# Performance work log

Hardware: AMD Instinct MI355X
Metric: run time of the kernel (lower is better)

The kernel has to match this reference:

```python
import jax, jax.numpy as jnp
import numpy as np
from jax import lax

B, C, N, NB = 64, 512, 1024, 4
BC = C // NB
KS = [3, 5, 7, 9]
LEVEL = 2  # min(2, pywt.dwt_max_level(1024, 8)) = 2
FL = 8  # db4 filter length
DN = ('NCH', 'OIH', 'NCH')
# pywt db4 decomposition filters
DEC_LO = jnp.array([-0.010597401784997278, 0.032883011666982945, 0.030841381835986965,
                    -0.18703481171888114, -0.02798376941698385, 0.6308807679295904,
                    0.7148465705525415, 0.23037781330885523], jnp.float32)
DEC_HI = jnp.array([-0.23037781330885523, 0.7148465705525415, -0.6308807679295904,
                    -0.02798376941698385, 0.18703481171888114, 0.030841381835986965,
                    -0.032883011666982945, -0.010597401784997278], jnp.float32)


def conv1d(x, w, b, pad):
    y = lax.conv_general_dilated(x, w, (1,), [(pad, pad)], dimension_numbers=DN)
    return y + b[None, :, None]


def bn_relu(x, g, beta, eps=1e-5):
    # BatchNorm1d in train mode: batch statistics over (B, L) per channel
    mu = x.mean(axis=(0, 2), keepdims=True)
    var = ((x - mu) ** 2).mean(axis=(0, 2), keepdims=True)
    xn = (x - mu) * lax.rsqrt(var + eps)
    return jax.nn.relu(xn * g[None, :, None] + beta[None, :, None])


def dwt1d(x):
    # single-level pywt-compatible DWT, symmetric mode. x: [B, C, n]
    b, c, n = x.shape
    out = (n + FL - 1) // 2
    p = 2 * (out - 1) - n + FL
    xp = jnp.pad(x, ((0, 0), (0, 0), (p // 2, p - p // 2)), mode='symmetric')
    k = jnp.stack([DEC_LO[::-1], DEC_HI[::-1]])[:, None, :]  # [2,1,FL]
    y = lax.conv_general_dilated(xp.reshape(b * c, 1, -1), k, (2,), 'VALID',
                                 dimension_numbers=DN)
    y = y.reshape(b, c, 2, out)
    return y[:, :, 0], y[:, :, 1]  # (cA, cD)


def idwt1d(lo, hi):
    # single-level inverse DWT; output length = 2*nc - FL + 2
    b, c, nc = lo.shape
    x = jnp.stack([lo, hi], axis=2).reshape(b * c, 2, nc)
    # rec filters = dec filters reversed, so flipped-for-conv == dec filters
    k = jnp.stack([DEC_LO, DEC_HI])[None, :, :]  # [1,2,FL]
    y = lax.conv_general_dilated(x, k, (1,), [(FL - 1, FL - 1)],
                                 lhs_dilation=(2,), dimension_numbers=DN)
    y = y[:, 0, FL - 2: FL - 2 + 2 * nc - FL + 2]
    return y.reshape(b, c, -1)


def decouple(x):
    # TemporalPatternDecoupling: db4 wavedec(level=2) -> reconstruct low-pass-only
    # (long term) and detail-only (short term). Torch detaches before pywt.
    x = lax.stop_gradient(x)
    n = x.shape[-1]
    a, details = x, []
    for _ in range(LEVEL):
        a, d = dwt1d(a)
        details.append(d)
    la, sa = a, jnp.zeros_like(a)
    for d in reversed(details):
        dl = d.shape[-1]
        la = idwt1d(la[..., :dl], jnp.zeros_like(d))
        sa = idwt1d(sa[..., :dl], d)
    return sa[..., :n], la[..., :n]


def setup_inputs() -> dict:
    key = jax.random.key(0)
    ks = jax.random.split(key, 32)
    s = 0.05
    inp = {
        'x': jax.random.normal(ks[0], (B, C, N), jnp.float32),
        'w_init': jax.random.normal(ks[1], (C, C, 1), jnp.float32) * s,
        'b_init': jnp.zeros((C,), jnp.float32),
        'w_pf': jax.random.normal(ks[2], (BC, 2 * BC, 1), jnp.float32) * s,
        'b_pf': jnp.zeros((BC,), jnp.float32),
        'w_fus': jax.random.normal(ks[3], (C, C, 1), jnp.float32) * s,
        'b_fus': jnp.zeros((C,), jnp.float32),
    }
    for i in range(NB):
        inp[f'w_b{i + 1}'] = jax.random.normal(ks[4 + i], (BC, BC, KS[i]), jnp.float32) * s
        inp[f'b_b{i + 1}'] = jnp.zeros((BC,), jnp.float32)
        inp[f'g_b{i + 1}'] = jnp.ones((BC,), jnp.float32)
        inp[f'be_b{i + 1}'] = jnp.zeros((BC,), jnp.float32)
    return inp


def reference(x, w_init, b_init, w_b1, b_b1, g_b1, be_b1, w_b2, b_b2, g_b2, be_b2,
              w_b3, b_b3, g_b3, be_b3, w_b4, b_b4, g_b4, be_b4, w_pf, b_pf,
              w_fus, b_fus):
    identity = x
    h = conv1d(x, w_init, b_init, 0)
    branch_in = jnp.split(h, NB, axis=1)
    wb = [w_b1, w_b2, w_b3, w_b4]
    bb = [b_b1, b_b2, b_b3, b_b4]
    gb = [g_b1, g_b2, g_b3, g_b4]
    beb = [be_b1, be_b2, be_b3, be_b4]
    shorts, longs = [], []
    for i in range(NB):
        y = bn_relu(conv1d(branch_in[i], wb[i], bb[i], KS[i] // 2), gb[i], beb[i])
        s, l = decouple(y)
        shorts.append(s)
        longs.append(l)
    for b in range(1, NB):
        shorts[b] = shorts[b] + shorts[b - 1]
    for b in range(NB - 2, -1, -1):
        longs[b] = longs[b] + longs[b + 1]
    enhanced = [conv1d(jnp.concatenate([shorts[b], longs[b]], axis=1), w_pf, b_pf, 0)
                for b in range(NB)]
    out = conv1d(jnp.concatenate(enhanced, axis=1), w_fus, b_fus, 0)
    return out + identity
```

## Files before the change

### kernel.cpp

```cpp
#include <hip/hip_runtime.h>

typedef float  f32x4 __attribute__((ext_vector_type(4)));
typedef short  s16x8 __attribute__((ext_vector_type(8)));
typedef short  s16x4 __attribute__((ext_vector_type(4)));
typedef unsigned short u16;

struct PtrQuad { const float* p[4]; };

__constant__ float c_lo[8] = {-0.010597401784997278f, 0.032883011666982945f,
                              0.030841381835986965f, -0.18703481171888114f,
                              -0.02798376941698385f, 0.6308807679295904f,
                              0.7148465705525415f,  0.23037781330885523f};
__constant__ float c_hi[8] = {-0.23037781330885523f, 0.7148465705525415f,
                              -0.6308807679295904f, -0.02798376941698385f,
                              0.18703481171888114f, 0.030841381835986965f,
                              -0.032883011666982945f, -0.010597401784997278f};

__device__ __forceinline__ u16 f2bf(float f) {
    unsigned u = __float_as_uint(f);
    u += 0x7fffu + ((u >> 16) & 1u);
    return (u16)(u >> 16);
}
__device__ __forceinline__ float bf2f(u16 h) {
    return __uint_as_float(((unsigned)h) << 16);
}
__device__ __forceinline__ int lds_chunk(int row, int g) {
    return row * 4 + (g ^ ((row >> 1) & 3));
}
__device__ __forceinline__ void gload16(void* lds, const void* g) {
    __builtin_amdgcn_global_load_lds(
        (__attribute__((address_space(1))) const void*)g,
        (__attribute__((address_space(3))) void*)lds,
        16, 0, 0);
}
__device__ __forceinline__ void pipe_wait2(int t, int nt) {
    if (t + 1 < nt) asm volatile("s_waitcnt vmcnt(4)" ::: "memory");
    else            asm volatile("s_waitcnt vmcnt(0)" ::: "memory");
    __builtin_amdgcn_s_barrier();
    __builtin_amdgcn_sched_barrier(0);
}
__device__ __forceinline__ void pipe_endbar() {
    __builtin_amdgcn_sched_barrier(0);
    __builtin_amdgcn_s_barrier();
}

__global__ __launch_bounds__(256) void gemm_nt_k(
    const u16* __restrict__ A, long aB, int lda,
    const u16* __restrict__ B, long bB, int ldb,
    int K,
    u16* __restrict__ D, long dB, int dj,
    const float* __restrict__ bias)
{
    __shared__ s16x8 As[2 * 512];
    __shared__ s16x8 Bs[2 * 512];
    int flat = blockIdx.x + 8 * (blockIdx.y + 4 * blockIdx.z);
    int swz = (flat & 7) * 256 + (flat >> 3);
    const int j0 = (swz & 7) * 128;
    const int i0 = ((swz >> 3) & 3) * 128;
    const long bb = swz >> 5;
    const u16* Ab = A + bb * aB;
    const u16* Bb = B + bb * bB;
    const int tid = threadIdx.x;
    const int srow = tid >> 2, sg = tid & 3;
    const int ssg = sg ^ ((srow >> 1) & 3);
    const int l = tid & 63, w = tid >> 6;
    const int wi = (w >> 1) * 64, wj = (w & 1) * 64;
    const int lr = l & 15, lg = l >> 4;
    const long aoff0 = (long)(i0 + srow) * lda + ssg * 8;
    const long aoff1 = (long)(i0 + srow + 64) * lda + ssg * 8;
    const long boff0 = (long)(j0 + srow) * ldb + ssg * 8;
    const long boff1 = (long)(j0 + srow + 64) * ldb + ssg * 8;
    const int nt = K >> 5;
    auto stage = [&](int buf, int t) {
        const int k0 = t << 5;
        char* a0 = (char*)As + buf * 8192 + w * 1024;
        char* b0 = (char*)Bs + buf * 8192 + w * 1024;
        gload16(a0, Ab + aoff0 + k0);
        gload16(a0 + 4096, Ab + aoff1 + k0);
        gload16(b0, Bb + boff0 + k0);
        gload16(b0 + 4096, Bb + boff1 + k0);
    };
    f32x4 acc[4][4] = {};
    stage(0, 0);
    for (int t = 0; t < nt; ++t) {
        const int cur = t & 1;
        if (t + 1 < nt) stage(cur ^ 1, t + 1);
        pipe_wait2(t, nt);
        s16x8 af[4], bf[4];
        #pragma unroll
        for (int f = 0; f < 4; ++f) {
            af[f] = As[cur * 512 + lds_chunk(wi + f * 16 + lr, lg)];
            bf[f] = Bs[cur * 512 + lds_chunk(wj + f * 16 + lr, lg)];
        }
        __builtin_amdgcn_s_setprio(1);
        #pragma unroll
        for (int fi = 0; fi < 4; ++fi)
            #pragma unroll
            for (int fj = 0; fj < 4; ++fj)
                acc[fi][fj] = __builtin_amdgcn_mfma_f32_16x16x32_bf16(af[fi], bf[fj], acc[fi][fj], 0, 0, 0);
        __builtin_amdgcn_s_setprio(0);
        pipe_endbar();
    }
    u16* Db = D + bb * dB;
    #pragma unroll
    for (int fi = 0; fi < 4; ++fi) {
        const int i = i0 + wi + fi * 16 + lg * 4;
        float b0 = 0, b1 = 0, b2v = 0, b3 = 0;
        if (bias) { b0 = bias[i]; b1 = bias[i + 1]; b2v = bias[i + 2]; b3 = bias[i + 3]; }
        #pragma unroll
        for (int fj = 0; fj < 4; ++fj) {
            const int j = j0 + wj + fj * 16 + lr;
            f32x4 d = acc[fi][fj];
            s16x4 o;
            o[0] = (short)f2bf(d[0] + b0); o[1] = (short)f2bf(d[1] + b1);
            o[2] = (short)f2bf(d[2] + b2v); o[3] = (short)f2bf(d[3] + b3);
            *(s16x4*)(Db + (long)j * dj + i) = o;
        }
    }
}

__global__ __launch_bounds__(256) void gemm_branch4_k(
    const u16* __restrict__ WpAll,
    const u16* __restrict__ H,
    u16* __restrict__ Y,
    const u16* __restrict__ zbuf,
    float* __restrict__ part)
{
    __shared__ char Alds[2 * 8192];
    __shared__ char Blds[2 * 12288];
    __shared__ float sred[2][128];
    __shared__ float qred[2][128];
    int flat = blockIdx.x + 8 * (blockIdx.y + 4 * blockIdx.z);
    int swz = (flat & 7) * 256 + (flat >> 3);
    const int jblk = swz & 7;
    const int br = (swz >> 3) & 3;
    const long bb = swz >> 5;
    const int j0 = jblk * 128;
    const int taps = 3 + 2 * br;
    const int pad = 1 + br;
    const u16* Wpb = WpAll + (long)(br * br + 2 * br) * 16384;
    const u16* Hb = H + bb * 524288 + 128 * br;
    const int tid = threadIdx.x;
    const int l = tid & 63, w = tid >> 6;
    const int wi = (w >> 1) * 64, wj = (w & 1) * 64;
    const int lr = l & 15, lg = l >> 4;
    const int lrow = l >> 2, lq = l & 3;
    const int ssg2 = lq ^ ((lrow >> 1) & 3);
    const int lda = taps * 128;

    auto stageA = [&](int buf, int c, int t) {
        char* dst = Alds + buf * 8192 + w * 2048;
        #pragma unroll
        for (int q = 0; q < 2; ++q) {
            int row = w * 32 + q * 16 + lrow;
            gload16(dst + q * 1024,
                    Wpb + (long)row * lda + t * 128 + c * 32 + ssg2 * 8);
        }
    };
    auto stageB = [&](int buf, int c) {
        char* dst = Blds + buf * 12288 + w * 3072;
        #pragma unroll
        for (int q = 0; q < 3; ++q) {
            int winrow = w * 48 + q * 16 + lrow;
            int grow = j0 - 32 + winrow;
            const u16* src = (grow >= 0 && grow < 1024)
                           ? (Hb + (long)grow * 512 + c * 32 + ssg2 * 8) : zbuf;
            gload16(dst + q * 1024, src);
        }
    };

    f32x4 acc[4][4] = {};
    int abuf = 0, bbuf = 0;
    stageB(0, 0);
    stageA(0, 0, 0);
    for (int c = 0; c < 4; ++c) {
        for (int t = 0; t < taps; ++t) {
            if (t + 1 < taps) {
                stageA(abuf ^ 1, c, t + 1);
                asm volatile("s_waitcnt vmcnt(2)" ::: "memory");
            } else if (c + 1 < 4) {
                stageB(bbuf ^ 1, c + 1);
                stageA(abuf ^ 1, c + 1, 0);
                asm volatile("s_waitcnt vmcnt(5)" ::: "memory");
            } else {
                asm volatile("s_waitcnt vmcnt(0)" ::: "memory");
            }
            __builtin_amdgcn_s_barrier();
            __builtin_amdgcn_sched_barrier(0);
            const char* Al = Alds + abuf * 8192;
            const char* Bl = Blds + bbuf * 12288;
            const int shift2 = t - pad + 32;
            s16x8 af[4], bf[4];
            #pragma unroll
            for (int f = 0; f < 4; ++f) {
                int arow = wi + f * 16 + lr;
                af[f] = *(const s16x8*)(Al + arow * 64 + (lg ^ ((arow >> 1) & 3)) * 16);
                int brow = wj + f * 16 + lr + shift2;
                bf[f] = *(const s16x8*)(Bl + brow * 64 + (lg ^ ((brow >> 1) & 3)) * 16);
            }
            __builtin_amdgcn_s_setprio(1);
            #pragma unroll
            for (int fi = 0; fi < 4; ++fi)
                #pragma unroll
                for (int fj = 0; fj < 4; ++fj)
                    acc[fi][fj] = __builtin_amdgcn_mfma_f32_16x16x32_bf16(af[fi], bf[fj], acc[fi][fj], 0, 0, 0);
            __builtin_amdgcn_s_setprio(0);
            __builtin_amdgcn_sched_barrier(0);
            __builtin_amdgcn_s_barrier();
            abuf ^= 1;
            if (t == taps - 1) bbuf ^= 1;
        }
    }
    u16* Db = Y + bb * 524288 + 128 * br;
    #pragma unroll
    for (int fi = 0; fi < 4; ++fi) {
        const int i = wi + fi * 16 + lg * 4;
        #pragma unroll
        for (int fj = 0; fj < 4; ++fj) {
            const int j = j0 + wj + fj * 16 + lr;
            f32x4 d = acc[fi][fj];
            s16x4 o;
            o[0] = (short)f2bf(d[0]); o[1] = (short)f2bf(d[1]);
            o[2] = (short)f2bf(d[2]); o[3] = (short)f2bf(d[3]);
            *(s16x4*)(Db + (long)j * 512 + i) = o;
        }
    }
    float sv[16], qv[16];
    #pragma unroll
    for (int fi = 0; fi < 4; ++fi)
        #pragma unroll
        for (int e = 0; e < 4; ++e) {
            float s = 0.f, q = 0.f;
            #pragma unroll
            for (int fj = 0; fj < 4; ++fj) { float d = acc[fi][fj][e]; s += d; q += d * d; }
            sv[fi * 4 + e] = s; qv[fi * 4 + e] = q;
        }
    #pragma unroll
    for (int m = 1; m < 16; m <<= 1) {
        #pragma unroll
        for (int r = 0; r < 16; ++r) {
            sv[r] += __shfl_xor(sv[r], m, 64);
            qv[r] += __shfl_xor(qv[r], m, 64);
        }
    }
    __syncthreads();
    if (lr == 0) {
        #pragma unroll
        for (int r = 0; r < 16; ++r) {
            int co = wi + (r >> 2) * 16 + lg * 4 + (r & 3);
            sred[w & 1][co] = sv[r];
            qred[w & 1][co] = qv[r];
        }
    }
    __syncthreads();
    if (tid < 128) {
        long blk = (long)br * 512 + bb * 8 + jblk;
        part[blk * 256 + tid]       = sred[0][tid] + sred[1][tid];
        part[blk * 256 + 128 + tid] = qred[0][tid] + qred[1][tid];
    }
}

__global__ __launch_bounds__(256) void gemm_psl_k(
    const u16* __restrict__ Ybn,
    const u16* __restrict__ Bmat,
    u16* __restrict__ PSL)
{
    __shared__ s16x8 As[2 * 512];
    __shared__ s16x8 Bs[2 * 512];
    int flat = blockIdx.x + 8 * (blockIdx.y + 8 * blockIdx.z);
    int swz = (flat & 7) * 512 + (flat >> 3);
    const int j0 = (swz & 7) * 128;
    const int i0 = ((swz >> 3) & 7) * 128;
    const long bb = swz >> 6;
    const int tid = threadIdx.x;
    const u16* Ab = Ybn + bb * 524288;
    const int srow = tid >> 2, sg = tid & 3;
    const int ssg = sg ^ ((srow >> 1) & 3);
    const int l = tid & 63, w = tid >> 6;
    const int wi = (w >> 1) * 64, wj = (w & 1) * 64;
    const int lr = l & 15, lg = l >> 4;
    const long aoff0 = (long)(i0 + srow) * 512 + ssg * 8;
    const long aoff1 = (long)(i0 + srow + 64) * 512 + ssg * 8;
    const long boff0 = (long)(j0 + srow) * 512 + ssg * 8;
    const long boff1 = (long)(j0 + srow + 64) * 512 + ssg * 8;
    const int nt = 16;
    auto stage = [&](int buf, int t) {
        const int k0 = t << 5;
        char* a0 = (char*)As + buf * 8192 + w * 1024;
        char* b0 = (char*)Bs + buf * 8192 + w * 1024;
        gload16(a0, Ab + aoff0 + k0);
        gload16(a0 + 4096, Ab + aoff1 + k0);
        gload16(b0, Bmat + boff0 + k0);
        gload16(b0 + 4096, Bmat + boff1 + k0);
    };
    f32x4 acc[4][4] = {};
    stage(0, 0);
    for (int t = 0; t < nt; ++t) {
        const int cur = t & 1;
        if (t + 1 < nt) stage(cur ^ 1, t + 1);
        pipe_wait2(t, nt);
        s16x8 af[4], bf[4];
        #pragma unroll
        for (int f = 0; f < 4; ++f) {
            af[f] = As[cur * 512 + lds_chunk(wi + f * 16 + lr, lg)];
            bf[f] = Bs[cur * 512 + lds_chunk(wj + f * 16 + lr, lg)];
        }
        __builtin_amdgcn_s_setprio(1);
        #pragma unroll
        for (int fi = 0; fi < 4; ++fi)
            #pragma unroll
            for (int fj = 0; fj < 4; ++fj)
                acc[fi][fj] = __builtin_amdgcn_mfma_f32_16x16x32_bf16(af[fi], bf[fj], acc[fi][fj], 0, 0, 0);
        __builtin_amdgcn_s_setprio(0);
        pipe_endbar();
    }
    u16* Db = PSL + bb * 1048576;
    #pragma unroll
    for (int fi = 0; fi < 4; ++fi) {
        const int i = i0 + wi + fi * 16 + lg * 4;
        #pragma unroll
        for (int fj = 0; fj < 4; ++fj) {
            const int j = j0 + wj + fj * 16 + lr;
            f32x4 d = acc[fi][fj];
            s16x4 o;
            o[0] = (short)f2bf(d[0]); o[1] = (short)f2bf(d[1]);
            o[2] = (short)f2bf(d[2]); o[3] = (short)f2bf(d[3]);
            *(s16x4*)(Db + (long)j * 1024 + i) = o;
        }
    }
}

__global__ __launch_bounds__(256) void gemm_time_k(
    const u16* __restrict__ MS,
    const u16* __restrict__ PSL,
    const float* __restrict__ b2, const u16* __restrict__ xbf,
    float* __restrict__ OUT)
{
    __shared__ s16x8 As[2 * 512];
    __shared__ s16x8 Bs[2 * 512];
    int flat = blockIdx.x + 4 * (blockIdx.y + 8 * blockIdx.z);
    int swz = (flat & 7) * 256 + (flat >> 3);
    const int j0 = (swz & 3) * 128;
    const int i0 = ((swz >> 2) & 7) * 128;
    const long bb = swz >> 5;
    const int tid = threadIdx.x;
    const int srow = tid >> 2, sg = tid & 3;
    const int ssg = sg ^ ((srow >> 1) & 3);
    const int l = tid & 63, w = tid >> 6;
    const int wi = (w >> 1) * 64, wj = (w & 1) * 64;
    const int lr = l & 15, lg = l >> 4;
    const int klo = (i0 - 32) > 0 ? (i0 - 32) : 0;
    const int khi = (i0 + 160) < 1024 ? (i0 + 160) : 1024;
    const int nt = (khi - klo) >> 5;
    const u16* B = PSL + bb * 1048576;
    auto stage = [&](int buf, int t) {
        const int k0 = klo + (t << 5);
        char* a0 = (char*)As + buf * 8192 + w * 1024;
        char* b0 = (char*)Bs + buf * 8192 + w * 1024;
        gload16(a0, MS + (long)(i0 + srow) * 1024 + k0 + ssg * 8);
        gload16(a0 + 4096, MS + (long)(i0 + srow + 64) * 1024 + k0 + ssg * 8);
        gload16(b0, B + (long)(j0 + srow) * 1024 + k0 + ssg * 8);
        gload16(b0 + 4096, B + (long)(j0 + srow + 64) * 1024 + k0 + ssg * 8);
    };
    f32x4 acc[4][4] = {};
    stage(0, 0);
    for (int t = 0; t < nt; ++t) {
        const int cur = t & 1;
        if (t + 1 < nt) stage(cur ^ 1, t + 1);
        pipe_wait2(t, nt);
        s16x8 af[4], bf[4];
        #pragma unroll
        for (int f = 0; f < 4; ++f) {
            af[f] = As[cur * 512 + lds_chunk(wi + f * 16 + lr, lg)];
            bf[f] = Bs[cur * 512 + lds_chunk(wj + f * 16 + lr, lg)];
        }
        __builtin_amdgcn_s_setprio(1);
        #pragma unroll
        for (int fi = 0; fi < 4; ++fi)
            #pragma unroll
            for (int fj = 0; fj < 4; ++fj)
                acc[fi][fj] = __builtin_amdgcn_mfma_f32_16x16x32_bf16(af[fi], bf[fj], acc[fi][fj], 0, 0, 0);
        __builtin_amdgcn_s_setprio(0);
        pipe_endbar();
    }
    float* Ob = OUT + bb * 524288;
    const u16* Xb = xbf + bb * 524288;
    const u16* PLb = PSL + bb * 1048576 + 524288;
    #pragma unroll
    for (int fi = 0; fi < 4; ++fi) {
        const int i = i0 + wi + fi * 16 + lg * 4;
        #pragma unroll
        for (int fj = 0; fj < 4; ++fj) {
            const int j = j0 + wj + fj * 16 + lr;
            const long a = (long)j * 1024 + i;
            f32x4 d = acc[fi][fj];
            const float bj = b2[j];
            s16x4 xv4 = *(const s16x4*)(Xb + a);
            s16x4 pl4 = *(const s16x4*)(PLb + a);
            f32x4 o;
            o[0] = d[0] + bj + bf2f((u16)xv4[0]) + bf2f((u16)pl4[0]);
            o[1] = d[1] + bj + bf2f((u16)xv4[1]) + bf2f((u16)pl4[1]);
            o[2] = d[2] + bj + bf2f((u16)xv4[2]) + bf2f((u16)pl4[2]);
            o[3] = d[3] + bj + bf2f((u16)xv4[3]) + bf2f((u16)pl4[3]);
            *(f32x4*)(Ob + a) = o;
        }
    }
}

__global__ __launch_bounds__(256) void build_M_k(u16* __restrict__ MS)
{
    __shared__ float a1[515], d1[515], a2[261], d2[261], sa1[515];
    const int r = blockIdx.x;
    const int t = threadIdx.x;
    for (int m = t; m < 515; m += 256) {
        float sa = 0.f, sd = 0.f;
        #pragma unroll
        for (int j = 0; j < 8; ++j) {
            int tt = 2 * m + 1 - j;
            tt = (tt < 0) ? (-tt - 1) : tt;
            tt = (tt >= 1024) ? (2047 - tt) : tt;
            if (tt == r) { sa += c_lo[j]; sd += c_hi[j]; }
        }
        a1[m] = sa; d1[m] = sd;
    }
    __syncthreads();
    for (int m = t; m < 261; m += 256) {
        float sa = 0.f, sd = 0.f;
        #pragma unroll
        for (int j = 0; j < 8; ++j) {
            int tt = 2 * m + 1 - j;
            tt = (tt < 0) ? (-tt - 1) : tt;
            tt = (tt >= 515) ? (1029 - tt) : tt;
            float v = a1[tt];
            sa += v * c_lo[j]; sd += v * c_hi[j];
        }
        a2[m] = sa; d2[m] = sd;
    }
    __syncthreads();
    for (int m = t; m < 515; m += 256) {
        float ss = 0.f;
        #pragma unroll
        for (int k = 0; k < 8; ++k) {
            int tt = m + k - 1;
            if (tt & 1) continue;
            int j = tt >> 1;
            if (j < 0 || j >= 261) continue;
            ss += c_hi[k] * d2[j];
        }
        sa1[m] = ss;
    }
    __syncthreads();
    for (int n = t; n < 1024; n += 256) {
        float ss = 0.f;
        #pragma unroll
        for (int k = 0; k < 8; ++k) {
            int tt = n + k - 1;
            if (tt & 1) continue;
            int j = tt >> 1;
            if (j < 0 || j >= 515) continue;
            ss += c_lo[k] * sa1[j] + c_hi[k] * d1[j];
        }
        MS[(long)n * 1024 + r] = f2bf(ss);
    }
}

__global__ __launch_bounds__(256) void pack_weights_k(
    const float* __restrict__ wi,
    const float* __restrict__ b1, const float* __restrict__ b2_,
    const float* __restrict__ b3, const float* __restrict__ b4,
    const float* __restrict__ wf, const float* __restrict__ bpf,
    const float* __restrict__ bfus,
    u16* __restrict__ Wi, u16* __restrict__ Wp,
    float* __restrict__ bias2, float* __restrict__ zbuf)
{
    int i = blockIdx.x * 256 + threadIdx.x;
    if (i < 262144) Wi[i] = f2bf(wi[i]);
    if (i < 393216) {
        int base, taps;
        const float* s;
        if (i < 49152)       { base = 0;      taps = 3; s = b1; }
        else if (i < 131072) { base = 49152;  taps = 5; s = b2_; }
        else if (i < 245760) { base = 131072; taps = 7; s = b3; }
        else                 { base = 245760; taps = 9; s = b4; }
        int rem = i - base;
        int stride = taps * 128;
        int co = rem / stride;
        int r2 = rem - co * stride;
        int tap = r2 >> 7, ci = r2 & 127;
        Wp[i] = f2bf(s[(long)(co * 128 + ci) * taps + tap]);
    }
    if (i < 512) {
        float s = bfus[i];
        for (int j = 0; j < 512; ++j) s += wf[(long)i * 512 + j] * bpf[j & 127];
        bias2[i] = s;
    }
    if (i >= 512 && i < 576) zbuf[i - 512] = 0.f;
}

__global__ __launch_bounds__(256) void make_Ucum_k(
    const float* __restrict__ wf, const float* __restrict__ wp,
    u16* __restrict__ UDUL)
{
    int gid = blockIdx.x * 256 + threadIdx.x;
    int co = gid >> 7, cc = gid & 127;
    float us[4], ul[4];
    #pragma unroll
    for (int b = 0; b < 4; ++b) {
        float s = 0.f, t = 0.f;
        for (int q = 0; q < 128; ++q) {
            float f = wf[(long)co * 512 + b * 128 + q];
            s += f * wp[q * 256 + cc];
            t += f * wp[q * 256 + 128 + cc];
        }
        us[b] = s; ul[b] = t;
    }
    float suf[4], pre[4];
    float acc = 0.f;
    for (int b = 3; b >= 0; --b) { acc += us[b]; suf[b] = acc; }
    acc = 0.f;
    for (int b = 0; b < 4; ++b) { acc += ul[b]; pre[b] = acc; }
    #pragma unroll
    for (int b = 0; b < 4; ++b) {
        UDUL[(long)co * 512 + b * 128 + cc]         = f2bf(suf[b] - pre[b]);
        UDUL[(long)(512 + co) * 512 + b * 128 + cc] = f2bf(pre[b]);
    }
}

__global__ __launch_bounds__(256) void trX_k(const float* __restrict__ x,
                                             u16* __restrict__ xcl,
                                             u16* __restrict__ xbf)
{
    __shared__ float sh[32][33];
    const int n0 = blockIdx.x * 32, c0 = blockIdx.y * 32;
    const long bb = blockIdx.z;
    const int tx = threadIdx.x, ty = threadIdx.y;
    const float* xb = x + bb * 524288;
    u16* ob = xcl + bb * 524288;
    u16* fb = xbf + bb * 524288;
    #pragma unroll
    for (int k = 0; k < 4; ++k) {
        float v = xb[(long)(c0 + ty + 8 * k) * 1024 + n0 + tx];
        sh[ty + 8 * k][tx] = v;
        fb[(long)(c0 + ty + 8 * k) * 1024 + n0 + tx] = f2bf(v);
    }
    __syncthreads();
    #pragma unroll
    for (int k = 0; k < 4; ++k)
        ob[(long)(n0 + ty + 8 * k) * 512 + c0 + tx] = f2bf(sh[tx][ty + 8 * k]);
}

__global__ __launch_bounds__(256) void bn_coef_k(
    const float* __restrict__ part, PtrQuad g, PtrQuad be, float* __restrict__ scsh)
{
    __shared__ float rs[256], rq[256];
    int c = blockIdx.x;
    int br = c >> 7, cc = c & 127;
    const float* pb = part + (long)br * 131072;
    int t = threadIdx.x;
    float s = pb[(2 * t) * 256 + cc]       + pb[(2 * t + 1) * 256 + cc];
    float q = pb[(2 * t) * 256 + 128 + cc] + pb[(2 * t + 1) * 256 + 128 + cc];
    rs[t] = s; rq[t] = q;
    __syncthreads();
    for (int off = 128; off > 0; off >>= 1) {
        if (t < off) { rs[t] += rs[t + off]; rq[t] += rq[t + off]; }
        __syncthreads();
    }
    if (t == 0) {
        float mu = rs[0] * (1.0f / 65536.0f);
        float var = rq[0] * (1.0f / 65536.0f) - mu * mu;
        float sc = g.p[br][cc] * rsqrtf(var + 1e-5f);
        scsh[c] = sc;
        scsh[512 + c] = be.p[br][cc] - mu * sc;
    }
}

__global__ __launch_bounds__(256) void bn_apply_k(
    u16* __restrict__ Y, const float* __restrict__ scsh)
{
    __shared__ float sc_[512];
    __shared__ float sh_[512];
    const int t = threadIdx.x;
    #pragma unroll
    for (int q = 0; q < 2; ++q) {
        sc_[t + q * 256] = scsh[t + q * 256];
        sh_[t + q * 256] = scsh[512 + t + q * 256];
    }
    __syncthreads();
    long gid = (long)blockIdx.x * 256 + t;
    long r = gid >> 6; int cg = (int)(gid & 63);
    u16* p = Y + r * 512 + cg * 8;
    s16x8 v = *(const s16x8*)p;
    #pragma unroll
    for (int e = 0; e < 8; ++e) {
        int c = cg * 8 + e;
        float f = bf2f((u16)v[e]) * sc_[c] + sh_[c];
        v[e] = (short)f2bf(f > 0.f ? f : 0.f);
    }
    *(s16x8*)p = v;
}

extern "C" void kernel_launch(void* const* d_in, const int* in_sizes, int n_in,
                              void* d_out, int out_size, void* d_ws, size_t ws_size,
                              hipStream_t stream)
{
    const float* x      = (const float*)d_in[0];
    const float* w_init = (const float*)d_in[1];
    const float* b_init = (const float*)d_in[2];
    const float* w_pf   = (const float*)d_in[3];
    const float* b_pf   = (const float*)d_in[4];
    const float* w_fus  = (const float*)d_in[5];
    const float* b_fus  = (const float*)d_in[6];
    const float *w_b[4];
    PtrQuad g, be;
    for (int i = 0; i < 4; ++i) {
        w_b[i]  = (const float*)d_in[7 + 4 * i];
        g.p[i]  = (const float*)d_in[9 + 4 * i];
        be.p[i] = (const float*)d_in[10 + 4 * i];
    }
    float* outf = (float*)d_out;

    char* p = (char*)d_ws;
    u16* xcl   = (u16*)p;  p += 67108864;
    u16* xbf   = (u16*)p;  p += 67108864;
    u16* h     = (u16*)p;  p += 67108864;
    u16* Y     = (u16*)p;  p += 67108864;
    u16* PSL   = (u16*)p;  p += 134217728;
    u16* Wi    = (u16*)p;  p += 524288;
    u16* Wp    = (u16*)p;  p += 786432;
    u16* UDUL  = (u16*)p;  p += 1048576;
    u16* MrowS = (u16*)p;  p += 2097152;
    float* b2  = (float*)p; p += 2048;
    float* zbuf= (float*)p; p += 256;
    float* scsh= (float*)p; p += 4096;
    float* part= (float*)p; p += 2097152;

    pack_weights_k<<<1536, 256, 0, stream>>>(w_init, w_b[0], w_b[1], w_b[2], w_b[3],
                                             w_fus, b_pf, b_fus, Wi, Wp, b2, zbuf);
    make_Ucum_k<<<256, 256, 0, stream>>>(w_fus, w_pf, UDUL);
    build_M_k<<<1024, 256, 0, stream>>>(MrowS);

    trX_k<<<dim3(32, 16, 64), dim3(32, 8), 0, stream>>>(x, xcl, xbf);

    gemm_nt_k<<<dim3(8, 4, 64), 256, 0, stream>>>(Wi, 0, 512, xcl, 524288, 512, 512,
                                                  h, 524288, 512, b_init);

    gemm_branch4_k<<<dim3(8, 4, 64), 256, 0, stream>>>(Wp, h, Y, (const u16*)zbuf, part);

    bn_coef_k<<<512, 256, 0, stream>>>(part, g, be, scsh);
    bn_apply_k<<<16384, 256, 0, stream>>>(Y, scsh);

    gemm_psl_k<<<dim3(8, 8, 64), 256, 0, stream>>>(Y, UDUL, PSL);

    gemm_time_k<<<dim3(4, 8, 64), 256, 0, stream>>>(MrowS, PSL, b2, xbf, outf);
}
```

Before: 481.0 us.

## Use 512-thread 256x128 GEMM tiles for init and PSL projections

Replaces the 128x128 256-thread GEMM with a generic 512-thread kernel that computes 256x128 output tiles, with eight waves sharing one B tile. Both the init conv GEMM and the PSL GEMM now go through this kernel, and the separate gemm_psl_k is removed. The larger tile is meant to cut global/LDS traffic per MFMA and halve the workgroup count. In exchange it uses more LDS per block, fewer workgroups for latency hiding, and a new vmcnt(3) wait scheme.

```diff
diff --git a/kernel.cpp b/kernel.cpp
--- a/kernel.cpp
+++ b/kernel.cpp
@@ -44,52 +44,60 @@
     __builtin_amdgcn_s_barrier();
 }
 
-__global__ __launch_bounds__(256) void gemm_nt_k(
+__global__ __launch_bounds__(512) void gemm_nt8_k(
     const u16* __restrict__ A, long aB, int lda,
     const u16* __restrict__ B, long bB, int ldb,
-    int K,
+    int nI, int nJ,
     u16* __restrict__ D, long dB, int dj,
     const float* __restrict__ bias)
 {
-    __shared__ s16x8 As[2 * 512];
+    __shared__ s16x8 As[2 * 1024];
     __shared__ s16x8 Bs[2 * 512];
-    int flat = blockIdx.x + 8 * (blockIdx.y + 4 * blockIdx.z);
-    int swz = (flat & 7) * 256 + (flat >> 3);
-    const int j0 = (swz & 7) * 128;
-    const int i0 = ((swz >> 3) & 3) * 128;
-    const long bb = swz >> 5;
+    int flat = blockIdx.x + gridDim.x * (blockIdx.y + gridDim.y * blockIdx.z);
+    int nwg = gridDim.x * gridDim.y * gridDim.z;
+    int swz = (flat & 7) * (nwg >> 3) + (flat >> 3);
+    const int jt = swz % nJ;
+    int rest = swz / nJ;
+    const int it = rest % nI;
+    const long bb = rest / nI;
+    const int i0 = it * 256, j0 = jt * 128;
     const u16* Ab = A + bb * aB;
     const u16* Bb = B + bb * bB;
     const int tid = threadIdx.x;
     const int srow = tid >> 2, sg = tid & 3;
     const int ssg = sg ^ ((srow >> 1) & 3);
     const int l = tid & 63, w = tid >> 6;
-    const int wi = (w >> 1) * 64, wj = (w & 1) * 64;
+    const int wi = (w >> 1) * 64;
+    const int wj = (w & 1) * 64;
     const int lr = l & 15, lg = l >> 4;
     const long aoff0 = (long)(i0 + srow) * lda + ssg * 8;
-    const long aoff1 = (long)(i0 + srow + 64) * lda + ssg * 8;
-    const long boff0 = (long)(j0 + srow) * ldb + ssg * 8;
-    const long boff1 = (long)(j0 + srow + 64) * ldb + ssg * 8;
-    const int nt = K >> 5;
+    const long aoff1 = (long)(i0 + srow + 128) * lda + ssg * 8;
+    const long boff  = (long)(j0 + srow) * ldb + ssg * 8;
+    const int nt = 16;
     auto stage = [&](int buf, int t) {
         const int k0 = t << 5;
-        char* a0 = (char*)As + buf * 8192 + w * 1024;
+        char* a0 = (char*)As + buf * 16384 + w * 1024;
         char* b0 = (char*)Bs + buf * 8192 + w * 1024;
         gload16(a0, Ab + aoff0 + k0);
-        gload16(a0 + 4096, Ab + aoff1 + k0);
-        gload16(b0, Bb + boff0 + k0);
-        gload16(b0 + 4096, Bb + boff1 + k0);
+        gload16(a0 + 8192, Ab + aoff1 + k0);
+        gload16(b0, Bb + boff + k0);
     };
     f32x4 acc[4][4] = {};
     stage(0, 0);
     for (int t = 0; t < nt; ++t) {
         const int cur = t & 1;
-        if (t + 1 < nt) stage(cur ^ 1, t + 1);
-        pipe_wait2(t, nt);
+        if (t + 1 < nt) {
+            stage(cur ^ 1, t + 1);
+            asm volatile("s_waitcnt vmcnt(3)" ::: "memory");
+        } else {
+            asm volatile("s_waitcnt vmcnt(0)" ::: "memory");
+        }
+        __builtin_amdgcn_s_barrier();
+        __builtin_amdgcn_sched_barrier(0);
         s16x8 af[4], bf[4];
         #pragma unroll
         for (int f = 0; f < 4; ++f) {
-            af[f] = As[cur * 512 + lds_chunk(wi + f * 16 + lr, lg)];
+            af[f] = As[cur * 1024 + lds_chunk(wi + f * 16 + lr, lg)];
             bf[f] = Bs[cur * 512 + lds_chunk(wj + f * 16 + lr, lg)];
         }
         __builtin_amdgcn_s_setprio(1);
@@ -260,76 +268,6 @@
     }
 }
 
-__global__ __launch_bounds__(256) void gemm_psl_k(
-    const u16* __restrict__ Ybn,
-    const u16* __restrict__ Bmat,
-    u16* __restrict__ PSL)
-{
-    __shared__ s16x8 As[2 * 512];
-    __shared__ s16x8 Bs[2 * 512];
-    int flat = blockIdx.x + 8 * (blockIdx.y + 8 * blockIdx.z);
-    int swz = (flat & 7) * 512 + (flat >> 3);
-    const int j0 = (swz & 7) * 128;
-    const int i0 = ((swz >> 3) & 7) * 128;
-    const long bb = swz >> 6;
-    const int tid = threadIdx.x;
-    const u16* Ab = Ybn + bb * 524288;
-    const int srow = tid >> 2, sg = tid & 3;
-    const int ssg = sg ^ ((srow >> 1) & 3);
-    const int l = tid & 63, w = tid >> 6;
-    const int wi = (w >> 1) * 64, wj = (w & 1) * 64;
-    const int lr = l & 15, lg = l >> 4;
-    const long aoff0 = (long)(i0 + srow) * 512 + ssg * 8;
-    const long aoff1 = (long)(i0 + srow + 64) * 512 + ssg * 8;
-    const long boff0 = (long)(j0 + srow) * 512 + ssg * 8;
-    const long boff1 = (long)(j0 + srow + 64) * 512 + ssg * 8;
-    const int nt = 16;
-    auto stage = [&](int buf, int t) {
-        const int k0 = t << 5;
-        char* a0 = (char*)As + buf * 8192 + w * 1024;
-        char* b0 = (char*)Bs + buf * 8192 + w * 1024;
-        gload16(a0, Ab + aoff0 + k0);
-        gload16(a0 + 4096, Ab + aoff1 + k0);
-        gload16(b0, Bmat + boff0 + k0);
-        gload16(b0 + 4096, Bmat + boff1 + k0);
-    };
-    f32x4 acc[4][4] = {};
-    stage(0, 0);
-    for (int t = 0; t < nt; ++t) {
-        const int cur = t & 1;
-        if (t + 1 < nt) stage(cur ^ 1, t + 1);
-        pipe_wait2(t, nt);
-        s16x8 af[4], bf[4];
-        #pragma unroll
-        for (int f = 0; f < 4; ++f) {
-            af[f] = As[cur * 512 + lds_chunk(wi + f * 16 + lr, lg)];
-            bf[f] = Bs[cur * 512 + lds_chunk(wj + f * 16 + lr, lg)];
-        }
-        __builtin_amdgcn_s_setprio(1);
-        #pragma unroll
-        for (int fi = 0; fi < 4; ++fi)
-            #pragma unroll
-            for (int fj = 0; fj < 4; ++fj)
-                acc[fi][fj] = __builtin_amdgcn_mfma_f32_16x16x32_bf16(af[fi], bf[fj], acc[fi][fj], 0, 0, 0);
-        __builtin_amdgcn_s_setprio(0);
-        pipe_endbar();
-    }
-    u16* Db = PSL + bb * 1048576;
-    #pragma unroll
-    for (int fi = 0; fi < 4; ++fi) {
-        const int i = i0 + wi + fi * 16 + lg * 4;
-        #pragma unroll
-        for (int fj = 0; fj < 4; ++fj) {
-            const int j = j0 + wj + fj * 16 + lr;
-            f32x4 d = acc[fi][fj];
-            s16x4 o;
-            o[0] = (short)f2bf(d[0]); o[1] = (short)f2bf(d[1]);
-            o[2] = (short)f2bf(d[2]); o[3] = (short)f2bf(d[3]);
-            *(s16x4*)(Db + (long)j * 1024 + i) = o;
-        }
-    }
-}
-
 __global__ __launch_bounds__(256) void gemm_time_k(
     const u16* __restrict__ MS,
     const u16* __restrict__ PSL,
@@ -641,15 +579,16 @@
 
     trX_k<<<dim3(32, 16, 64), dim3(32, 8), 0, stream>>>(x, xcl, xbf);
 
-    gemm_nt_k<<<dim3(8, 4, 64), 256, 0, stream>>>(Wi, 0, 512, xcl, 524288, 512, 512,
-                                                  h, 524288, 512, b_init);
+    gemm_nt8_k<<<dim3(8, 2, 64), 512, 0, stream>>>(Wi, 0, 512, xcl, 524288, 512,
+                                                   2, 8, h, 524288, 512, b_init);
 
     gemm_branch4_k<<<dim3(8, 4, 64), 256, 0, stream>>>(Wp, h, Y, (const u16*)zbuf, part);
 
     bn_coef_k<<<512, 256, 0, stream>>>(part, g, be, scsh);
     bn_apply_k<<<16384, 256, 0, stream>>>(Y, scsh);
 
-    gemm_psl_k<<<dim3(8, 8, 64), 256, 0, stream>>>(Y, UDUL, PSL);
+    gemm_nt8_k<<<dim3(8, 4, 64), 512, 0, stream>>>(Y, 524288, 512, UDUL, 0, 512,
+                                                   4, 8, PSL, 1048576, 1024, nullptr);
 
     gemm_time_k<<<dim3(4, 8, 64), 256, 0, stream>>>(MrowS, PSL, b2, xbf, outf);
 }
```

New measurement: 516.6 us. 7.4% more time.
